# Optimization experiments

Measured on AMD Instinct MI355X. Metric: run time of the kernel, lower is better.

The kernel has to match this reference:

```python
import jax, jax.numpy as jnp
import numpy as np

EPS = 1e-8


def householder_matrix(vs, dim):
    """Sequentially apply Householder reflections: Q <- (I - 2 v v^T / ||v||^2) Q."""
    def body(Q, v):
        coef = 2.0 / (jnp.sum(v * v) + EPS)
        Q = Q - coef * jnp.outer(v, v @ Q)
        return Q, None
    Q0 = jnp.eye(dim, dtype=vs.dtype)
    Q, _ = jax.lax.scan(body, Q0, vs)
    return Q


def _rotate_half(x):
    x1, x2 = jnp.split(x, 2, axis=-1)
    return jnp.concatenate((-x2, x1), axis=-1)


def setup_inputs() -> dict:
    key = jax.random.key(0)
    kq, kk, kc, ks, kv = jax.random.split(key, 5)
    B, H, S, D = 4, 16, 4096, 64
    q = jax.random.normal(kq, (B, H, S, D), dtype=jnp.float32)
    k = jax.random.normal(kk, (B, H, S, D), dtype=jnp.float32)
    cos = jax.random.uniform(kc, (B, S, D), dtype=jnp.float32)
    sin = jax.random.uniform(ks, (B, S, D), dtype=jnp.float32)
    vs = jax.random.normal(kv, (D // 2, D), dtype=jnp.float32) * 0.02
    return {"q": q, "k": k, "cos": cos, "sin": sin, "vs": vs}


def reference(q, k, cos, sin, vs):
    D = q.shape[-1]
    Q = householder_matrix(vs, D)            # [D, D], orthogonal
    # inverse rotation: x @ Q^T
    qi = q @ Q.T
    ki = k @ Q.T
    cos_b = cos[:, None, :, :]               # [B,1,S,D]
    sin_b = sin[:, None, :, :]
    q_rot = qi * cos_b + _rotate_half(qi) * sin_b
    k_rot = ki * cos_b + _rotate_half(ki) * sin_b
    # forward rotation: x @ Q
    return q_rot @ Q, k_rot @ Q
```

## Files before the change

kernel.cpp:

```cpp
#include <hip/hip_runtime.h>

typedef __attribute__((ext_vector_type(8))) short short8;
typedef __attribute__((ext_vector_type(4))) float floatx4;
typedef unsigned short u16;
typedef unsigned int   u32;

__device__ __forceinline__ u32 f2bf(float f) {
  u32 u = __float_as_uint(f);
  return (u + 0x7fffu + ((u >> 16) & 1u)) >> 16;
}

__device__ __forceinline__ short8 cvt8(const float* f) {
  short8 r;
#pragma unroll
  for (int j = 0; j < 8; j++) r[j] = (short)f2bf(f[j]);
  return r;
}

__global__ void __launch_bounds__(64) hh_kernel(const float* __restrict__ vs,
                                                u16* __restrict__ Qb,
                                                u16* __restrict__ Qtb) {
  const int j = threadIdx.x;
  float col[64];
#pragma unroll
  for (int i = 0; i < 64; i++) col[i] = (i == j) ? 1.f : 0.f;

  __shared__ float v[64];
#pragma unroll 1
  for (int r = 0; r < 32; r++) {
    __syncthreads();
    v[j] = vs[r * 64 + j];
    __syncthreads();
    float vv0 = 0, vv1 = 0, vv2 = 0, vv3 = 0, w0 = 0, w1 = 0, w2 = 0, w3 = 0;
#pragma unroll
    for (int i = 0; i < 64; i += 4) {
      float a0 = v[i], a1 = v[i + 1], a2 = v[i + 2], a3 = v[i + 3];
      vv0 += a0 * a0; vv1 += a1 * a1; vv2 += a2 * a2; vv3 += a3 * a3;
      w0 += a0 * col[i]; w1 += a1 * col[i + 1]; w2 += a2 * col[i + 2]; w3 += a3 * col[i + 3];
    }
    float coef = 2.f / (((vv0 + vv1) + (vv2 + vv3)) + 1e-8f);
    float cw = coef * ((w0 + w1) + (w2 + w3));
#pragma unroll
    for (int i = 0; i < 64; i++) col[i] -= v[i] * cw;
  }
#pragma unroll
  for (int i = 0; i < 64; i++) {
    Qb [i * 64 + j] = (u16)f2bf(col[i]);
    Qtb[j * 64 + i] = (u16)f2bf(col[i]);
  }
}

__global__ void __launch_bounds__(256) rnrope_kernel(
    const float* __restrict__ qp, const float* __restrict__ kp,
    const float* __restrict__ cosp, const float* __restrict__ sinp,
    const u16* __restrict__ Qb, const u16* __restrict__ Qtb,
    float* __restrict__ outp) {
  const int lane = threadIdx.x & 63;
  const int t    = lane & 15;
  const int quad = lane >> 4;
  const int wave = blockIdx.x * 4 + (threadIdx.x >> 6);

  __shared__ alignas(16) u16 sh_all[4][1152];
  u16* sh = sh_all[threadIdx.x >> 6];

  short8 aQ[4][2], aT[4][2];
#pragma unroll
  for (int i0 = 0; i0 < 4; i0++) {
#pragma unroll
    for (int ks = 0; ks < 2; ks++) {
      aQ[i0][ks] = *(const short8*)(Qb  + (i0 * 16 + t) * 64 + ks * 32 + quad * 8);
      aT[i0][ks] = *(const short8*)(Qtb + (i0 * 16 + t) * 64 + ks * 32 + quad * 8);
    }
  }

#pragma unroll 1
  for (int it = 0; it < 4; ++it) {
    const int tile = wave * 4 + it;
    const int tt   = tile & 16383;
    const bool isq = (tile < 16384);
    const float* __restrict__ inp = isq ? qp : kp;
    float* __restrict__ op = outp + (isq ? 0 : 16777216);
    const int token_base = tt * 16;
    const int s = token_base & 4095;
    const int b = token_base >> 16;
    const int csoff = ((b << 12) + s + t) * 64;
    const float* crow = cosp + csoff;
    const float* srow = sinp + csoff;
    const float* xrow = inp + (token_base + t) * 64;

    float xb[16];
    *(float4*)&xb[0]  = *(const float4*)(xrow + quad * 8);
    *(float4*)&xb[4]  = *(const float4*)(xrow + quad * 8 + 4);
    *(float4*)&xb[8]  = *(const float4*)(xrow + 32 + quad * 8);
    *(float4*)&xb[12] = *(const float4*)(xrow + 32 + quad * 8 + 4);
    short8 bq0 = cvt8(&xb[0]);
    short8 bq1 = cvt8(&xb[8]);

    floatx4 acc[4];
#pragma unroll
    for (int i0 = 0; i0 < 4; i0++) {
      floatx4 z = {0.f, 0.f, 0.f, 0.f};
      z = __builtin_amdgcn_mfma_f32_16x16x32_bf16(aQ[i0][0], bq0, z, 0, 0, 0);
      z = __builtin_amdgcn_mfma_f32_16x16x32_bf16(aQ[i0][1], bq1, z, 0, 0, 0);
      acc[i0] = z;
    }

    float4 c[4], sn[4];
#pragma unroll
    for (int i0 = 0; i0 < 4; i0++) {
      c [i0] = *(const float4*)(crow + i0 * 16 + quad * 4);
      sn[i0] = *(const float4*)(srow + i0 * 16 + quad * 4);
    }

#pragma unroll
    for (int i0 = 0; i0 < 4; i0++) {
      const int p = i0 ^ 2;
      const float sg = (i0 < 2) ? -1.f : 1.f;
      float r0 = acc[i0][0] * c[i0].x + sg * acc[p][0] * sn[i0].x;
      float r1 = acc[i0][1] * c[i0].y + sg * acc[p][1] * sn[i0].y;
      float r2 = acc[i0][2] * c[i0].z + sg * acc[p][2] * sn[i0].z;
      float r3 = acc[i0][3] * c[i0].w + sg * acc[p][3] * sn[i0].w;
      u32 lo = f2bf(r0) | (f2bf(r1) << 16);
      u32 hi = f2bf(r2) | (f2bf(r3) << 16);
      *(uint2*)&sh[t * 72 + i0 * 16 + quad * 4] = make_uint2(lo, hi);
    }

    __builtin_amdgcn_wave_barrier();
    short8 br0 = *(const short8*)&sh[t * 72 + quad * 8];
    short8 br1 = *(const short8*)&sh[t * 72 + 32 + quad * 8];

#pragma unroll
    for (int o0 = 0; o0 < 4; o0++) {
      floatx4 z = {0.f, 0.f, 0.f, 0.f};
      z = __builtin_amdgcn_mfma_f32_16x16x32_bf16(aT[o0][0], br0, z, 0, 0, 0);
      z = __builtin_amdgcn_mfma_f32_16x16x32_bf16(aT[o0][1], br1, z, 0, 0, 0);
      float4 st = make_float4(z[0], z[1], z[2], z[3]);
      *(float4*)(op + (token_base + t) * 64 + o0 * 16 + quad * 4) = st;
    }
    __builtin_amdgcn_wave_barrier();
  }
}

extern "C" void kernel_launch(void* const* d_in, const int* in_sizes, int n_in,
                              void* d_out, int out_size, void* d_ws, size_t ws_size,
                              hipStream_t stream) {
  const float* q    = (const float*)d_in[0];
  const float* k    = (const float*)d_in[1];
  const float* cosp = (const float*)d_in[2];
  const float* sinp = (const float*)d_in[3];
  const float* vs   = (const float*)d_in[4];
  float* out = (float*)d_out;
  u16* Qb  = (u16*)d_ws;
  u16* Qtb = Qb + 4096;

  hipLaunchKernelGGL(hh_kernel, dim3(1), dim3(64), 0, stream, vs, Qb, Qtb);
  hipLaunchKernelGGL(rnrope_kernel, dim3(2048), dim3(256), 0, stream,
                     q, k, cosp, sinp, Qb, Qtb, out);
}
```

Before: 308.5 us.

## Process one tile per wave with a 4x larger grid and early loads

Drops the per-wave loop over four tiles and launches four times as many blocks, so each wave handles a single 16-token tile. All global loads for x, cos and sin are issued up front, before the Q fragments are fetched, to hide latency. Qt fragments are now loaded just before the second MFMA instead of being held in registers, and launch bounds ask for 5 blocks per CU to raise occupancy. The LDS row stride shrinks from 72 to 66, which saves shared memory but may change bank-conflict behaviour, and Q/Qt are now reloaded per tile rather than reused across four tiles.

```diff
diff --git a/kernel.cpp b/kernel.cpp
--- a/kernel.cpp
+++ b/kernel.cpp
@@ -50,7 +50,7 @@
   }
 }
 
-__global__ void __launch_bounds__(256) rnrope_kernel(
+__global__ void __launch_bounds__(256, 5) rnrope_kernel(
     const float* __restrict__ qp, const float* __restrict__ kp,
     const float* __restrict__ cosp, const float* __restrict__ sinp,
     const u16* __restrict__ Qb, const u16* __restrict__ Qtb,
@@ -58,86 +58,81 @@
   const int lane = threadIdx.x & 63;
   const int t    = lane & 15;
   const int quad = lane >> 4;
-  const int wave = blockIdx.x * 4 + (threadIdx.x >> 6);
+  const int widx = threadIdx.x >> 6;
+  const int tile = blockIdx.x * 4 + widx;
 
-  __shared__ alignas(16) u16 sh_all[4][1152];
-  u16* sh = sh_all[threadIdx.x >> 6];
+  __shared__ alignas(16) u16 sh_all[4][1056];
+  u16* sh = sh_all[widx];
 
-  short8 aQ[4][2], aT[4][2];
+  const int tt   = tile & 16383;
+  const bool isq = (tile < 16384);
+  const float* __restrict__ inp = isq ? qp : kp;
+  float* __restrict__ op = outp + (isq ? 0 : 16777216);
+  const int token_base = tt * 16;
+  const int s = token_base & 4095;
+  const int b = token_base >> 16;
+  const float* crow = cosp + ((b << 12) + s + t) * 64;
+  const float* srow = sinp + ((b << 12) + s + t) * 64;
+  const float* xrow = inp + (token_base + t) * 64;
+
+  float xb[16];
+  *(float4*)&xb[0]  = *(const float4*)(xrow + quad * 8);
+  *(float4*)&xb[4]  = *(const float4*)(xrow + quad * 8 + 4);
+  *(float4*)&xb[8]  = *(const float4*)(xrow + 32 + quad * 8);
+  *(float4*)&xb[12] = *(const float4*)(xrow + 32 + quad * 8 + 4);
+
+  float4 c[4], sn[4];
+#pragma unroll
+  for (int i0 = 0; i0 < 4; i0++) {
+    c [i0] = *(const float4*)(crow + i0 * 16 + quad * 4);
+    sn[i0] = *(const float4*)(srow + i0 * 16 + quad * 4);
+  }
+
+  short8 aQ[4][2];
 #pragma unroll
   for (int i0 = 0; i0 < 4; i0++) {
 #pragma unroll
-    for (int ks = 0; ks < 2; ks++) {
-      aQ[i0][ks] = *(const short8*)(Qb  + (i0 * 16 + t) * 64 + ks * 32 + quad * 8);
-      aT[i0][ks] = *(const short8*)(Qtb + (i0 * 16 + t) * 64 + ks * 32 + quad * 8);
-    }
+    for (int ks = 0; ks < 2; ks++)
+      aQ[i0][ks] = *(const short8*)(Qb + (i0 * 16 + t) * 64 + ks * 32 + quad * 8);
   }
 
-#pragma unroll 1
-  for (int it = 0; it < 4; ++it) {
-    const int tile = wave * 4 + it;
-    const int tt   = tile & 16383;
-    const bool isq = (tile < 16384);
-    const float* __restrict__ inp = isq ? qp : kp;
-    float* __restrict__ op = outp + (isq ? 0 : 16777216);
-    const int token_base = tt * 16;
-    const int s = token_base & 4095;
-    const int b = token_base >> 16;
-    const int csoff = ((b << 12) + s + t) * 64;
-    const float* crow = cosp + csoff;
-    const float* srow = sinp + csoff;
-    const float* xrow = inp + (token_base + t) * 64;
-
-    float xb[16];
-    *(float4*)&xb[0]  = *(const float4*)(xrow + quad * 8);
-    *(float4*)&xb[4]  = *(const float4*)(xrow + quad * 8 + 4);
-    *(float4*)&xb[8]  = *(const float4*)(xrow + 32 + quad * 8);
-    *(float4*)&xb[12] = *(const float4*)(xrow + 32 + quad * 8 + 4);
-    short8 bq0 = cvt8(&xb[0]);
-    short8 bq1 = cvt8(&xb[8]);
-
-    floatx4 acc[4];
+  short8 bq0 = cvt8(&xb[0]);
+  short8 bq1 = cvt8(&xb[8]);
+  floatx4 acc[4];
 #pragma unroll
-    for (int i0 = 0; i0 < 4; i0++) {
-      floatx4 z = {0.f, 0.f, 0.f, 0.f};
-      z = __builtin_amdgcn_mfma_f32_16x16x32_bf16(aQ[i0][0], bq0, z, 0, 0, 0);
-      z = __builtin_amdgcn_mfma_f32_16x16x32_bf16(aQ[i0][1], bq1, z, 0, 0, 0);
-      acc[i0] = z;
-    }
-
-    float4 c[4], sn[4];
-#pragma unroll
-    for (int i0 = 0; i0 < 4; i0++) {
-      c [i0] = *(const float4*)(crow + i0 * 16 + quad * 4);
-      sn[i0] = *(const float4*)(srow + i0 * 16 + quad * 4);
-    }
+  for (int i0 = 0; i0 < 4; i0++) {
+    floatx4 z = {0.f, 0.f, 0.f, 0.f};
+    z = __builtin_amdgcn_mfma_f32_16x16x32_bf16(aQ[i0][0], bq0, z, 0, 0, 0);
+    z = __builtin_amdgcn_mfma_f32_16x16x32_bf16(aQ[i0][1], bq1, z, 0, 0, 0);
+    acc[i0] = z;
+  }
 
 #pragma unroll
-    for (int i0 = 0; i0 < 4; i0++) {
-      const int p = i0 ^ 2;
-      const float sg = (i0 < 2) ? -1.f : 1.f;
-      float r0 = acc[i0][0] * c[i0].x + sg * acc[p][0] * sn[i0].x;
-      float r1 = acc[i0][1] * c[i0].y + sg * acc[p][1] * sn[i0].y;
-      float r2 = acc[i0][2] * c[i0].z + sg * acc[p][2] * sn[i0].z;
-      float r3 = acc[i0][3] * c[i0].w + sg * acc[p][3] * sn[i0].w;
-      u32 lo = f2bf(r0) | (f2bf(r1) << 16);
-      u32 hi = f2bf(r2) | (f2bf(r3) << 16);
-      *(uint2*)&sh[t * 72 + i0 * 16 + quad * 4] = make_uint2(lo, hi);
-    }
+  for (int i0 = 0; i0 < 4; i0++) {
+    const int p = i0 ^ 2;
+    const float sg = (i0 < 2) ? -1.f : 1.f;
+    float r0 = acc[i0][0] * c[i0].x + sg * acc[p][0] * sn[i0].x;
+    float r1 = acc[i0][1] * c[i0].y + sg * acc[p][1] * sn[i0].y;
+    float r2 = acc[i0][2] * c[i0].z + sg * acc[p][2] * sn[i0].z;
+    float r3 = acc[i0][3] * c[i0].w + sg * acc[p][3] * sn[i0].w;
+    u32 lo = f2bf(r0) | (f2bf(r1) << 16);
+    u32 hi = f2bf(r2) | (f2bf(r3) << 16);
+    *(uint2*)&sh[t * 66 + i0 * 16 + quad * 4] = make_uint2(lo, hi);
+  }
 
-    __builtin_amdgcn_wave_barrier();
-    short8 br0 = *(const short8*)&sh[t * 72 + quad * 8];
-    short8 br1 = *(const short8*)&sh[t * 72 + 32 + quad * 8];
+  __builtin_amdgcn_wave_barrier();
+  short8 br0 = *(const short8*)&sh[t * 66 + quad * 8];
+  short8 br1 = *(const short8*)&sh[t * 66 + 32 + quad * 8];
 
 #pragma unroll
-    for (int o0 = 0; o0 < 4; o0++) {
-      floatx4 z = {0.f, 0.f, 0.f, 0.f};
-      z = __builtin_amdgcn_mfma_f32_16x16x32_bf16(aT[o0][0], br0, z, 0, 0, 0);
-      z = __builtin_amdgcn_mfma_f32_16x16x32_bf16(aT[o0][1], br1, z, 0, 0, 0);
-      float4 st = make_float4(z[0], z[1], z[2], z[3]);
-      *(float4*)(op + (token_base + t) * 64 + o0 * 16 + quad * 4) = st;
-    }
-    __builtin_amdgcn_wave_barrier();
+  for (int o0 = 0; o0 < 4; o0++) {
+    short8 aT0 = *(const short8*)(Qtb + (o0 * 16 + t) * 64 + quad * 8);
+    short8 aT1 = *(const short8*)(Qtb + (o0 * 16 + t) * 64 + 32 + quad * 8);
+    floatx4 z = {0.f, 0.f, 0.f, 0.f};
+    z = __builtin_amdgcn_mfma_f32_16x16x32_bf16(aT0, br0, z, 0, 0, 0);
+    z = __builtin_amdgcn_mfma_f32_16x16x32_bf16(aT1, br1, z, 0, 0, 0);
+    *(float4*)(op + (token_base + t) * 64 + o0 * 16 + quad * 4) =
+        make_float4(z[0], z[1], z[2], z[3]);
   }
 }
 
@@ -154,6 +149,6 @@
   u16* Qtb = Qb + 4096;
 
   hipLaunchKernelGGL(hh_kernel, dim3(1), dim3(64), 0, stream, vs, Qb, Qtb);
-  hipLaunchKernelGGL(rnrope_kernel, dim3(2048), dim3(256), 0, stream,
+  hipLaunchKernelGGL(rnrope_kernel, dim3(8192), dim3(256), 0, stream,
                      q, k, cosp, sinp, Qb, Qtb, out);
 }
```

Measured after the change: 324.4 us. +5.1%, slower.
